# Optimization experiments

Measured on AMD Instinct MI355X. Metric: run time of the kernel, lower is better.

The kernel has to match this reference:

```python
import jax, jax.numpy as jnp
import numpy as np

BIG = 1000000.0


def setup_inputs() -> dict:
    key = jax.random.key(0)
    k1, k2 = jax.random.split(key)
    embeddings = jax.random.normal(k1, (8192, 128), dtype=jnp.float32)
    labels = jax.random.randint(k2, (8192,), 0, 512, dtype=jnp.int64)
    return {"embeddings": embeddings, "labels": labels, "margin": jnp.float32(0.5)}


def _pairwise_euclidean(x):
    # [N, N] Euclidean distance matrix, numerically safe sqrt (zero diag)
    sq = jnp.sum(x * x, axis=1)
    d2 = sq[:, None] + sq[None, :] - 2.0 * (x @ x.T)
    d2 = jnp.maximum(d2, 0.0)
    nz = d2 > 0.0
    return jnp.where(nz, jnp.sqrt(jnp.where(nz, d2, 1.0)), 0.0)


def reference(embeddings, labels, margin):
    n = embeddings.shape[0]
    dist = _pairwise_euclidean(embeddings)                      # [N, N]
    same = (labels[:, None] == labels[None, :]).astype(dist.dtype)
    mask_pos = same - jnp.eye(n, dtype=dist.dtype)              # positives, excl. self
    mask_neg = 1.0 - same                                       # different label
    pos_dist = jnp.max(dist * mask_pos, axis=1)                 # hardest positive
    neg_dist = jnp.min(dist + (1.0 - mask_neg) * BIG, axis=1)   # hardest negative
    loss = jax.nn.relu(pos_dist - neg_dist + margin)
    return jnp.mean(loss)
```

## Files before the change

kernel.cpp:

```cpp
#include <hip/hip_runtime.h>
#include <hip/hip_bf16.h>

#define NROW 8192
#define DIM  128
#define BI   128
#define BJ   128
#define JSPLIT 8
#define LSTR 136
#define BIGF 1e30f

typedef __attribute__((ext_vector_type(8))) short bf16x8;
typedef __attribute__((ext_vector_type(4))) float f32x4;


__device__ __forceinline__ unsigned short f2bf(float f) {
    unsigned u = __float_as_uint(f);
    unsigned r = (u + 0x7fffu + ((u >> 16) & 1u)) >> 16;
    return (unsigned short)r;
}

__global__ __launch_bounds__(256) void prep_kernel(const float* __restrict__ x,
                                                   unsigned short* __restrict__ xb,
                                                   float* __restrict__ sq,
                                                   unsigned* __restrict__ posb,
                                                   unsigned* __restrict__ negb,
                                                   float* __restrict__ out) {
    int gtid = blockIdx.x * 256 + threadIdx.x;
    if (gtid < NROW) {
        posb[gtid] = 0u;
        negb[gtid] = __float_as_uint(BIGF);
    }
    if (gtid == 0) out[0] = 0.0f;
    int row  = gtid >> 6;
    int lane = threadIdx.x & 63;
    const float* xr = x + (size_t)row * DIM;
    float a = xr[lane];
    float b = xr[lane + 64];
    xb[(size_t)row * DIM + lane]      = f2bf(a);
    xb[(size_t)row * DIM + lane + 64] = f2bf(b);
    float s = a * a + b * b;
    #pragma unroll
    for (int o = 32; o > 0; o >>= 1) s += __shfl_down(s, o);
    if (lane == 0) sq[row] = s;
}

__global__ __launch_bounds__(256, 2) void tri_mfma(const unsigned short* __restrict__ xb,
                                                   const int* __restrict__ lbl,
                                                   const float* __restrict__ sq,
                                                   unsigned* __restrict__ posb,
                                                   unsigned* __restrict__ negb) {
    __shared__ unsigned short As[BI * LSTR];
    __shared__ unsigned short Bs[BJ * LSTR];

    const int bid = blockIdx.x;
    const int rb  = bid >> 3;
    const int jq  = bid & 7;
    const int i0  = rb * BI;
    const int t    = threadIdx.x;
    const int lane = t & 63;
    const int w    = t >> 6;
    const int wrow = (w >> 1) * 64;
    const int wcol = (w & 1) * 64;
    const int quad = lane >> 4;
    const int l15  = lane & 15;

    {
        const int srow = t >> 4;
        const int schk = t & 15;
        #pragma unroll
        for (int it = 0; it < 8; it++) {
            int row = srow + it * 16;
            uint4 v = *(const uint4*)(xb + (size_t)(i0 + row) * DIM + schk * 8);
            *(uint4*)(&As[row * LSTR + schk * 8]) = v;
        }
    }

    float sqi[4][4];
    int   lbli[4][4];
    #pragma unroll
    for (int ti = 0; ti < 4; ti++) {
        int rbase = i0 + wrow + ti * 16 + quad * 4;
        float4 s4 = *(const float4*)(sq + rbase);
        int4   l4 = *(const int4*)(lbl + rbase);
        sqi[ti][0] = s4.x; sqi[ti][1] = s4.y; sqi[ti][2] = s4.z; sqi[ti][3] = s4.w;
        lbli[ti][0] = l4.x; lbli[ti][1] = l4.y; lbli[ti][2] = l4.z; lbli[ti][3] = l4.w;
    }

    float posm[4][4], negm[4][4];
    #pragma unroll
    for (int ti = 0; ti < 4; ti++)
        #pragma unroll
        for (int r = 0; r < 4; r++) { posm[ti][r] = -BIGF; negm[ti][r] = BIGF; }

    #pragma unroll 1
    for (int jt = 0; jt < (NROW / JSPLIT) / BJ; jt++) {
        const int j0 = jq * (NROW / JSPLIT) + jt * BJ;
        __syncthreads();
        {
            const int srow = t >> 4;
            const int schk = t & 15;
            #pragma unroll
            for (int it = 0; it < 8; it++) {
                int row = srow + it * 16;
                uint4 v = *(const uint4*)(xb + (size_t)(j0 + row) * DIM + schk * 8);
                *(uint4*)(&Bs[row * LSTR + schk * 8]) = v;
            }
        }
        __syncthreads();

        float sqj[4]; int lblj[4];
        #pragma unroll
        for (int tj = 0; tj < 4; tj++) {
            int c = j0 + wcol + tj * 16 + l15;
            sqj[tj]  = sq[c];
            lblj[tj] = lbl[c];
        }

        f32x4 acc[4][4];
        #pragma unroll
        for (int ti = 0; ti < 4; ti++)
            #pragma unroll
            for (int tj = 0; tj < 4; tj++) acc[ti][tj] = (f32x4){0.f, 0.f, 0.f, 0.f};

        #pragma unroll
        for (int ks = 0; ks < 4; ks++) {
            bf16x8 af[4], bfr[4];
            #pragma unroll
            for (int ti = 0; ti < 4; ti++)
                af[ti] = *(const bf16x8*)(&As[(wrow + ti * 16 + l15) * LSTR + ks * 32 + quad * 8]);
            #pragma unroll
            for (int tj = 0; tj < 4; tj++)
                bfr[tj] = *(const bf16x8*)(&Bs[(wcol + tj * 16 + l15) * LSTR + ks * 32 + quad * 8]);
            #pragma unroll
            for (int ti = 0; ti < 4; ti++)
                #pragma unroll
                for (int tj = 0; tj < 4; tj++)
                    acc[ti][tj] = __builtin_amdgcn_mfma_f32_16x16x32_bf16(af[ti], bfr[tj], acc[ti][tj], 0, 0, 0);
        }

        const bool diag = (i0 + wrow) == (j0 + wcol);
        #pragma unroll
        for (int ti = 0; ti < 4; ti++)
            #pragma unroll
            for (int tj = 0; tj < 4; tj++)
                #pragma unroll
                for (int r = 0; r < 4; r++) {
                    float s = fmaf(-2.0f, acc[ti][tj][r], sqj[tj]);
                    bool same = (lbli[ti][r] == lblj[tj]);
                    bool isd  = diag && (ti == tj) && (quad * 4 + r == l15);
                    float sp = (same && !isd) ? s : -BIGF;
                    float sn = same ? BIGF : s;
                    posm[ti][r] = fmaxf(posm[ti][r], sp);
                    negm[ti][r] = fminf(negm[ti][r], sn);
                }
    }

    #pragma unroll
    for (int ti = 0; ti < 4; ti++)
        #pragma unroll
        for (int r = 0; r < 4; r++) {
            float p = posm[ti][r];
            float n = negm[ti][r];
            #pragma unroll
            for (int m = 8; m >= 1; m >>= 1) {
                p = fmaxf(p, __shfl_xor(p, m));
                n = fminf(n, __shfl_xor(n, m));
            }
            if (l15 == 0) {
                int row = i0 + wrow + ti * 16 + quad * 4 + r;
                float d2p = fmaxf(0.0f, sqi[ti][r] + p);
                float d2n = fmaxf(0.0f, sqi[ti][r] + n);
                atomicMax(&posb[row], __float_as_uint(d2p));
                atomicMin(&negb[row], __float_as_uint(d2n));
            }
        }
}

__global__ __launch_bounds__(256) void tri_final(const unsigned* __restrict__ posb,
                                                 const unsigned* __restrict__ negb,
                                                 const float* __restrict__ margin,
                                                 float* __restrict__ out) {
    int r = blockIdx.x * 256 + threadIdx.x;
    float m = margin[0];
    float p  = sqrtf(__uint_as_float(posb[r]));
    float ng = sqrtf(__uint_as_float(negb[r]));
    float loss = fmaxf(p - ng + m, 0.0f) * (1.0f / (float)NROW);
    #pragma unroll
    for (int o = 32; o > 0; o >>= 1) loss += __shfl_down(loss, o);
    __shared__ float wsum[4];
    int lane = threadIdx.x & 63, wv = threadIdx.x >> 6;
    if (lane == 0) wsum[wv] = loss;
    __syncthreads();
    if (threadIdx.x == 0) atomicAdd(out, wsum[0] + wsum[1] + wsum[2] + wsum[3]);
}

extern "C" void kernel_launch(void* const* d_in, const int* in_sizes, int n_in,
                              void* d_out, int out_size, void* d_ws, size_t ws_size,
                              hipStream_t stream) {
    const float* x      = (const float*)d_in[0];
    const int*   lbl    = (const int*)d_in[1];
    const float* margin = (const float*)d_in[2];
    float* out = (float*)d_out;

    unsigned short* xb = (unsigned short*)d_ws;
    float*    sq   = (float*)((char*)d_ws + (size_t)NROW * DIM * 2);
    unsigned* posb = (unsigned*)((char*)sq + NROW * 4);
    unsigned* negb = posb + NROW;

    prep_kernel<<<2048, 256, 0, stream>>>(x, xb, sq, posb, negb, out);
    tri_mfma<<<64 * JSPLIT, 256, 0, stream>>>(xb, lbl, sq, posb, negb);
    tri_final<<<NROW / 256, 256, 0, stream>>>(posb, negb, margin, out);
}
```

Measured before the change: 90.68 us.

## Pre-swizzle bf16 embeddings into MFMA fragment layout and drop LDS staging

The prep kernel now writes the bf16 embeddings in a per-16-row-tile layout that matches the MFMA operand fragments, and packs squared norm and label into one 8-byte meta record. The main kernel then loads A and B fragments straight from global memory into registers, which removes shared memory staging and the two barriers per tile. The diagonal-exclusion test is split into its own branch so ordinary tiles skip it. The cost is that each wave now fetches its own B fragments, so the L2 traffic is duplicated across the two waves sharing a column, and register pressure rises with 16 held A fragments.

```diff
diff --git a/kernel.cpp b/kernel.cpp
--- a/kernel.cpp
+++ b/kernel.cpp
@@ -3,10 +3,7 @@
 
 #define NROW 8192
 #define DIM  128
-#define BI   128
-#define BJ   128
 #define JSPLIT 8
-#define LSTR 136
 #define BIGF 1e30f
 
 typedef __attribute__((ext_vector_type(8))) short bf16x8;
@@ -20,8 +17,9 @@
 }
 
 __global__ __launch_bounds__(256) void prep_kernel(const float* __restrict__ x,
-                                                   unsigned short* __restrict__ xb,
-                                                   float* __restrict__ sq,
+                                                   const int* __restrict__ lbl,
+                                                   unsigned short* __restrict__ xbT,
+                                                   uint2* __restrict__ meta,
                                                    unsigned* __restrict__ posb,
                                                    unsigned* __restrict__ negb,
                                                    float* __restrict__ out) {
@@ -31,31 +29,45 @@
         negb[gtid] = __float_as_uint(BIGF);
     }
     if (gtid == 0) out[0] = 0.0f;
-    int row  = gtid >> 6;
+
+    int wave = gtid >> 6;
     int lane = threadIdx.x & 63;
-    const float* xr = x + (size_t)row * DIM;
-    float a = xr[lane];
-    float b = xr[lane + 64];
-    xb[(size_t)row * DIM + lane]      = f2bf(a);
-    xb[(size_t)row * DIM + lane + 64] = f2bf(b);
-    float s = a * a + b * b;
-    #pragma unroll
-    for (int o = 32; o > 0; o >>= 1) s += __shfl_down(s, o);
-    if (lane == 0) sq[row] = s;
-}
-
-__global__ __launch_bounds__(256, 2) void tri_mfma(const unsigned short* __restrict__ xb,
-                                                   const int* __restrict__ lbl,
-                                                   const float* __restrict__ sq,
+    int q = lane >> 4, l = lane & 15;
+    int row = wave * 16 + l;
+    const float* xr = x + (size_t)row * DIM + q * 8;
+
+    float s = 0.0f;
+    #pragma unroll
+    for (int ks = 0; ks < 4; ks++) {
+        float4 a = *(const float4*)(xr + ks * 32);
+        float4 b = *(const float4*)(xr + ks * 32 + 4);
+        s += a.x * a.x + a.y * a.y + a.z * a.z + a.w * a.w;
+        s += b.x * b.x + b.y * b.y + b.z * b.z + b.w * b.w;
+        uint4 u;
+        u.x = (unsigned)f2bf(a.x) | ((unsigned)f2bf(a.y) << 16);
+        u.y = (unsigned)f2bf(a.z) | ((unsigned)f2bf(a.w) << 16);
+        u.z = (unsigned)f2bf(b.x) | ((unsigned)f2bf(b.y) << 16);
+        u.w = (unsigned)f2bf(b.z) | ((unsigned)f2bf(b.w) << 16);
+        *(uint4*)(xbT + (size_t)wave * 2048 + ks * 512 + lane * 8) = u;
+    }
+    s += __shfl_xor(s, 16);
+    s += __shfl_xor(s, 32);
+    if (q == 0) {
+        uint2 mv;
+        mv.x = __float_as_uint(s);
+        mv.y = (unsigned)lbl[row];
+        meta[row] = mv;
+    }
+}
+
+__global__ __launch_bounds__(256, 2) void tri_mfma(const unsigned short* __restrict__ xbT,
+                                                   const uint2* __restrict__ meta,
                                                    unsigned* __restrict__ posb,
                                                    unsigned* __restrict__ negb) {
-    __shared__ unsigned short As[BI * LSTR];
-    __shared__ unsigned short Bs[BJ * LSTR];
-
-    const int bid = blockIdx.x;
-    const int rb  = bid >> 3;
-    const int jq  = bid & 7;
-    const int i0  = rb * BI;
+    const int bid  = blockIdx.x;
+    const int rb   = bid >> 3;
+    const int jq   = bid & 7;
+    const int i0   = rb * 128;
     const int t    = threadIdx.x;
     const int lane = t & 63;
     const int w    = t >> 6;
@@ -64,26 +76,26 @@
     const int quad = lane >> 4;
     const int l15  = lane & 15;
 
+    bf16x8 A[4][4];
     {
-        const int srow = t >> 4;
-        const int schk = t & 15;
-        #pragma unroll
-        for (int it = 0; it < 8; it++) {
-            int row = srow + it * 16;
-            uint4 v = *(const uint4*)(xb + (size_t)(i0 + row) * DIM + schk * 8);
-            *(uint4*)(&As[row * LSTR + schk * 8]) = v;
-        }
-    }
-
-    float sqi[4][4];
-    int   lbli[4][4];
+        const int tbase = (i0 + wrow) >> 4;
+        #pragma unroll
+        for (int ti = 0; ti < 4; ti++)
+            #pragma unroll
+            for (int ks = 0; ks < 4; ks++)
+                A[ti][ks] = *(const bf16x8*)(xbT + ((size_t)(tbase + ti) * 2048 + ks * 512 + lane * 8));
+    }
+
+    float sqi[4][4]; int lbli[4][4];
     #pragma unroll
     for (int ti = 0; ti < 4; ti++) {
         int rbase = i0 + wrow + ti * 16 + quad * 4;
-        float4 s4 = *(const float4*)(sq + rbase);
-        int4   l4 = *(const int4*)(lbl + rbase);
-        sqi[ti][0] = s4.x; sqi[ti][1] = s4.y; sqi[ti][2] = s4.z; sqi[ti][3] = s4.w;
-        lbli[ti][0] = l4.x; lbli[ti][1] = l4.y; lbli[ti][2] = l4.z; lbli[ti][3] = l4.w;
+        uint4 m01 = *(const uint4*)(meta + rbase);
+        uint4 m23 = *(const uint4*)(meta + rbase + 2);
+        sqi[ti][0] = __uint_as_float(m01.x); lbli[ti][0] = (int)m01.y;
+        sqi[ti][1] = __uint_as_float(m01.z); lbli[ti][1] = (int)m01.w;
+        sqi[ti][2] = __uint_as_float(m23.x); lbli[ti][2] = (int)m23.y;
+        sqi[ti][3] = __uint_as_float(m23.z); lbli[ti][3] = (int)m23.w;
     }
 
     float posm[4][4], negm[4][4];
@@ -92,29 +104,28 @@
         #pragma unroll
         for (int r = 0; r < 4; r++) { posm[ti][r] = -BIGF; negm[ti][r] = BIGF; }
 
+    const int jbase = jq * (NROW / JSPLIT);
+    const int dr    = l15 - quad * 4;
+
     #pragma unroll 1
-    for (int jt = 0; jt < (NROW / JSPLIT) / BJ; jt++) {
-        const int j0 = jq * (NROW / JSPLIT) + jt * BJ;
-        __syncthreads();
-        {
-            const int srow = t >> 4;
-            const int schk = t & 15;
-            #pragma unroll
-            for (int it = 0; it < 8; it++) {
-                int row = srow + it * 16;
-                uint4 v = *(const uint4*)(xb + (size_t)(j0 + row) * DIM + schk * 8);
-                *(uint4*)(&Bs[row * LSTR + schk * 8]) = v;
-            }
+    for (int jt = 0; jt < (NROW / JSPLIT) / 128; jt++) {
+        const int j0 = jbase + jt * 128;
+        const int tb = (j0 + wcol) >> 4;
+
+        bf16x8 Bv[4][4];
+        #pragma unroll
+        for (int tj = 0; tj < 4; tj++)
+            #pragma unroll
+            for (int ks = 0; ks < 4; ks++)
+                Bv[tj][ks] = *(const bf16x8*)(xbT + ((size_t)(tb + tj) * 2048 + ks * 512 + lane * 8));
+
+        float sqj[4]; int lblj[4];
+        #pragma unroll
+        for (int tj = 0; tj < 4; tj++) {
+            uint2 mv = meta[j0 + wcol + tj * 16 + l15];
+            sqj[tj]  = __uint_as_float(mv.x);
+            lblj[tj] = (int)mv.y;
         }
-        __syncthreads();
-
-        float sqj[4]; int lblj[4];
-        #pragma unroll
-        for (int tj = 0; tj < 4; tj++) {
-            int c = j0 + wcol + tj * 16 + l15;
-            sqj[tj]  = sq[c];
-            lblj[tj] = lbl[c];
-        }
 
         f32x4 acc[4][4];
         #pragma unroll
@@ -123,36 +134,40 @@
             for (int tj = 0; tj < 4; tj++) acc[ti][tj] = (f32x4){0.f, 0.f, 0.f, 0.f};
 
         #pragma unroll
-        for (int ks = 0; ks < 4; ks++) {
-            bf16x8 af[4], bfr[4];
-            #pragma unroll
-            for (int ti = 0; ti < 4; ti++)
-                af[ti] = *(const bf16x8*)(&As[(wrow + ti * 16 + l15) * LSTR + ks * 32 + quad * 8]);
-            #pragma unroll
-            for (int tj = 0; tj < 4; tj++)
-                bfr[tj] = *(const bf16x8*)(&Bs[(wcol + tj * 16 + l15) * LSTR + ks * 32 + quad * 8]);
+        for (int ks = 0; ks < 4; ks++)
             #pragma unroll
             for (int ti = 0; ti < 4; ti++)
                 #pragma unroll
                 for (int tj = 0; tj < 4; tj++)
-                    acc[ti][tj] = __builtin_amdgcn_mfma_f32_16x16x32_bf16(af[ti], bfr[tj], acc[ti][tj], 0, 0, 0);
+                    acc[ti][tj] = __builtin_amdgcn_mfma_f32_16x16x32_bf16(A[ti][ks], Bv[tj][ks], acc[ti][tj], 0, 0, 0);
+
+        const bool diag = (i0 + wrow) == (j0 + wcol);
+        if (!diag) {
+            #pragma unroll
+            for (int ti = 0; ti < 4; ti++)
+                #pragma unroll
+                for (int tj = 0; tj < 4; tj++)
+                    #pragma unroll
+                    for (int r = 0; r < 4; r++) {
+                        float s = fmaf(-2.0f, acc[ti][tj][r], sqj[tj]);
+                        bool same = (lbli[ti][r] == lblj[tj]);
+                        posm[ti][r] = fmaxf(posm[ti][r], same ? s : -BIGF);
+                        negm[ti][r] = fminf(negm[ti][r], same ? BIGF : s);
+                    }
+        } else {
+            #pragma unroll
+            for (int ti = 0; ti < 4; ti++)
+                #pragma unroll
+                for (int tj = 0; tj < 4; tj++)
+                    #pragma unroll
+                    for (int r = 0; r < 4; r++) {
+                        float s = fmaf(-2.0f, acc[ti][tj][r], sqj[tj]);
+                        bool same = (lbli[ti][r] == lblj[tj]);
+                        bool isd  = (ti == tj) && (dr == r);
+                        posm[ti][r] = fmaxf(posm[ti][r], (same && !isd) ? s : -BIGF);
+                        negm[ti][r] = fminf(negm[ti][r], same ? BIGF : s);
+                    }
         }
-
-        const bool diag = (i0 + wrow) == (j0 + wcol);
-        #pragma unroll
-        for (int ti = 0; ti < 4; ti++)
-            #pragma unroll
-            for (int tj = 0; tj < 4; tj++)
-                #pragma unroll
-                for (int r = 0; r < 4; r++) {
-                    float s = fmaf(-2.0f, acc[ti][tj][r], sqj[tj]);
-                    bool same = (lbli[ti][r] == lblj[tj]);
-                    bool isd  = diag && (ti == tj) && (quad * 4 + r == l15);
-                    float sp = (same && !isd) ? s : -BIGF;
-                    float sn = same ? BIGF : s;
-                    posm[ti][r] = fmaxf(posm[ti][r], sp);
-                    negm[ti][r] = fminf(negm[ti][r], sn);
-                }
     }
 
     #pragma unroll
@@ -202,12 +217,12 @@
     const float* margin = (const float*)d_in[2];
     float* out = (float*)d_out;
 
-    unsigned short* xb = (unsigned short*)d_ws;
-    float*    sq   = (float*)((char*)d_ws + (size_t)NROW * DIM * 2);
-    unsigned* posb = (unsigned*)((char*)sq + NROW * 4);
+    unsigned short* xbT = (unsigned short*)d_ws;
+    uint2*    meta = (uint2*)((char*)d_ws + (size_t)NROW * DIM * 2);
+    unsigned* posb = (unsigned*)((char*)meta + NROW * 8);
     unsigned* negb = posb + NROW;
 
-    prep_kernel<<<2048, 256, 0, stream>>>(x, xb, sq, posb, negb, out);
-    tri_mfma<<<64 * JSPLIT, 256, 0, stream>>>(xb, lbl, sq, posb, negb);
+    prep_kernel<<<128, 256, 0, stream>>>(x, lbl, xbT, meta, posb, negb, out);
+    tri_mfma<<<64 * JSPLIT, 256, 0, stream>>>(xbT, meta, posb, negb);
     tri_final<<<NROW / 256, 256, 0, stream>>>(posb, negb, margin, out);
 }
```

Result: slower. 93.06 us (+2.6%).
